# Performance work log

Measured on AMD Instinct MI355X. Metric: run time of the kernel, lower is better.

Reference implementation:

```python
import jax, jax.numpy as jnp
import numpy as np
from jax import lax

N, L, D, P, H, QK, VP = 1, 512, 256, 128, 8, 8, 8
FIN = H * P + H * VP * 7 + H * 7  # 1528: pair + value-point + beta features


def _l2g(R, t, p):
    # local_to_global: q = R @ p + t, applied over flattened point dims
    s = p.shape
    p3 = p.reshape(s[0], s[1], -1, 3)
    q = jnp.einsum('nlij,nlmj->nlmi', R, p3) + t[:, :, None, :]
    return q.reshape(s)


def _g2l(R, t, q):
    # global_to_local: p = R^T @ (q - t)
    s = q.shape
    q3 = q.reshape(s[0], s[1], -1, 3)
    p = jnp.einsum('nlji,nlmj->nlmi', R, q3 - t[:, :, None, :])
    return p.reshape(s)


def _inorm(x):  # InstanceNorm2d, affine=False, eps=1e-5, NCHW
    m = x.mean(axis=(2, 3), keepdims=True)
    v = x.var(axis=(2, 3), keepdims=True)
    return (x - m) * lax.rsqrt(v + 1e-5)


def _conv3(x, w, b):  # 3x3, stride 1, pad 1
    y = lax.conv_general_dilated(x, w, (1, 1), [(1, 1), (1, 1)],
                                 dimension_numbers=('NCHW', 'OIHW', 'NCHW'))
    return y + b[None, :, None, None]


def _ln(x, g, b):  # LayerNorm over last dim, eps=1e-5
    m = x.mean(-1, keepdims=True)
    v = x.var(-1, keepdims=True)
    return (x - m) * lax.rsqrt(v + 1e-5) * g + b


def _leaky(x):  # LeakyReLU, negative_slope=0.01
    return jnp.where(x >= 0, x, 0.01 * x)


def setup_inputs():
    key = jax.random.key(0)
    ks = jax.random.split(key, 24)
    s = 0.05
    return {
        'R': jax.random.normal(ks[0], (N, L, 3, 3), jnp.float32),
        't': jax.random.normal(ks[1], (N, L, 3), jnp.float32),
        'p_CB': jax.random.normal(ks[2], (N, L, 3), jnp.float32),
        'x': jax.random.normal(ks[3], (N, L, D), jnp.float32),
        'z': jax.random.normal(ks[4], (N, L, L, P), jnp.float32),
        'W_p2h': jax.random.normal(ks[5], (P, H), jnp.float32) * s,
        'gamma': jnp.ones((1, 1, H), jnp.float32),
        'Wq': jax.random.normal(ks[6], (D, H * QK * 3), jnp.float32) * s,
        'Wk': jax.random.normal(ks[7], (D, H * QK * 3), jnp.float32) * s,
        'Wv': jax.random.normal(ks[8], (D, H * VP * 3), jnp.float32) * s,
        'W1': jax.random.normal(ks[9], (FIN, 2 * D), jnp.float32) * s,
        'b1': jnp.zeros((2 * D,), jnp.float32),
        'ln1_g': jnp.ones((2 * D,), jnp.float32),
        'ln1_b': jnp.zeros((2 * D,), jnp.float32),
        'W2': jax.random.normal(ks[10], (2 * D, D), jnp.float32) * s,
        'b2': jnp.zeros((D,), jnp.float32),
        'ca_w': jax.random.normal(ks[11], (H, 2 * H, 3, 3), jnp.float32) * s,
        'ca_b': jnp.zeros((H,), jnp.float32),
        'ln_g': jnp.ones((D,), jnp.float32),
        'ln_b': jnp.zeros((D,), jnp.float32),
        'cp_w': jax.random.normal(ks[12], (P, H + P, 3, 3), jnp.float32) * s,
        'cp_b': jnp.zeros((P,), jnp.float32),
        'mask': jnp.ones((N, L), dtype=bool),
    }


def reference(R, t, p_CB, x, z, W_p2h, gamma, Wq, Wk, Wv, W1, b1, ln1_g, ln1_b,
              W2, b2, ca_w, ca_b, ln_g, ln_b, cp_w, cp_b, mask):
    n, l = x.shape[:2]
    # pair logits [n,l,l,H]
    logits_pair = jnp.einsum('nijp,ph->nijh', z, W_p2h)
    # spatial (point) logits: squared distances between global q/k points
    q_s = _l2g(R, t, (x @ Wq).reshape(n, l, H * QK, 3)).reshape(n, l, H, QK * 3)
    k_s = _l2g(R, t, (x @ Wk).reshape(n, l, H * QK, 3)).reshape(n, l, H, QK * 3)
    ssd = ((q_s ** 2).sum(-1)[:, :, None, :] + (k_s ** 2).sum(-1)[:, None, :, :]
           - 2.0 * jnp.einsum('nihd,njhd->nijh', q_s, k_s))
    logits_spatial = ssd * (-gamma * jnp.sqrt(2.0 / (9.0 * QK)) / 2.0)
    # conv2dalpha: InstanceNorm -> 3x3 conv -> LeakyReLU over the LxL grid
    lg = jnp.concatenate([logits_pair, logits_spatial], axis=-1).transpose(0, 3, 1, 2)
    logits_sum = _leaky(_conv3(_inorm(lg), ca_w, ca_b)).transpose(0, 2, 3, 1)
    mask_row = mask[:, :, None, None]
    mask_pair = mask_row & mask[:, None, :, None]
    logits_sum = jnp.where(mask_pair, logits_sum, logits_sum - 1e6)
    alpha = jax.nn.softmax(logits_sum, axis=2)
    alpha = jnp.where(mask_row, alpha, 0.0)
    # pair aggregation [n,l,H*P]
    feat_p2n = jnp.einsum('nijh,nijp->nihp', alpha, z).reshape(n, l, H * P)
    # spatial (value point) aggregation
    v_pts = _l2g(R, t, (x @ Wv).reshape(n, l, H, VP, 3))
    aggr = jnp.einsum('nijh,njhvc->nihvc', alpha, v_pts)
    fp = _g2l(R, t, aggr)  # [n,l,H,VP,3]
    fn = jnp.sqrt((fp ** 2).sum(-1))
    fdir = fp / (fn[..., None] + 1e-6)
    feat_spatial = jnp.concatenate(
        [fp.reshape(n, l, -1), fn.reshape(n, l, -1), fdir.reshape(n, l, -1)], -1)
    # beta (CB point) aggregation
    aggr_b = jnp.einsum('nijh,njc->nihc', alpha, p_CB)
    fpb = _g2l(R, t, aggr_b)  # [n,l,H,3]
    fnb = jnp.sqrt((fpb ** 2).sum(-1))
    fdb = fpb / (fnb[..., None] + 1e-6)
    feat_beta = jnp.concatenate([fpb.reshape(n, l, -1), fnb, fdb.reshape(n, l, -1)], -1)
    # out_transform: Linear -> LayerNorm -> LeakyReLU -> Linear
    feat_all = jnp.concatenate([feat_p2n, feat_spatial, feat_beta], -1)
    h1 = _leaky(_ln(feat_all @ W1 + b1, ln1_g, ln1_b))
    fa = h1 @ W2 + b2
    fa = jnp.where(mask[..., None], fa, 0.0)
    x_out = _ln(x + fa, ln_g, ln_b)
    # alpha2pair: InstanceNorm -> 3x3 conv -> LeakyReLU
    pz = jnp.concatenate([z, alpha], -1).transpose(0, 3, 1, 2)
    pair_out = _leaky(_conv3(_inorm(pz), cp_w, cp_b)).transpose(0, 2, 3, 1)
    return (x_out, pair_out)
```

## Files before the change

kernel.cpp:

```cpp
#include <hip/hip_runtime.h>
#include <hip/hip_bf16.h>
#include <math.h>

#define Lr 512
#define LL (512*512)
#define PZROW 73728

typedef __bf16 bf16x8 __attribute__((ext_vector_type(8)));
typedef float f32x16 __attribute__((ext_vector_type(16)));

static __device__ __forceinline__ unsigned short f2bf(float f) {
    union { float f; unsigned u; } a; a.f = f;
    unsigned r = a.u + 0x7fff + ((a.u >> 16) & 1);
    return (unsigned short)(r >> 16);
}

static __device__ __forceinline__ unsigned pack2(float lo, float hi) {
    return (unsigned)f2bf(lo) | ((unsigned)f2bf(hi) << 16);
}

__global__ __launch_bounds__(512) void zero_stats_k(float* lg_acc, float* pz_acc) {
    int t = threadIdx.x;
    if (t < 32) lg_acc[t] = 0.f;
    if (t < 272) pz_acc[t] = 0.f;
}

__global__ __launch_bounds__(256) void wb_prep_k(const float* __restrict__ cpw,
        const float* __restrict__ pzmr, unsigned short* __restrict__ wb) {
    int idx = blockIdx.x * 256 + threadIdx.x;
    if (idx >= 128 * 1296) return;
    int j = idx & 7;
    int n = (idx >> 3) & 127;
    int rest = idx >> 10;
    int lhi = rest & 1;
    int ksn = (rest >> 1) % 9;
    int tap = rest / 18;
    int c = ksn * 16 + lhi * 8 + j;
    float v = (c < 136) ? cpw[(n * 136 + c) * 9 + tap] * pzmr[c * 2 + 1] : 0.f;
    wb[idx] = f2bf(v);
}

__global__ __launch_bounds__(128) void kc_prep_k(const float* __restrict__ cpw,
        const float* __restrict__ pzmr, float* __restrict__ kc) {
    int idx = blockIdx.x * 128 + threadIdx.x;
    if (idx >= 1152) return;
    int o = idx / 9, tap = idx % 9;
    float s = 0.f;
    for (int c = 0; c < 136; c++)
        s += cpw[(o * 136 + c) * 9 + tap] * pzmr[c * 2 + 1] * pzmr[c * 2];
    kc[idx] = -s;
}

__device__ __forceinline__ const float* qkv_colptr(const float* Wq, const float* Wk, const float* Wv, int c) {
    return c < 192 ? (Wq + c) : (c < 384 ? (Wk + c - 192) : (Wv + c - 384));
}

__global__ __launch_bounds__(256) void qkv_k(const float* __restrict__ x,
        const float* __restrict__ Wq, const float* __restrict__ Wk, const float* __restrict__ Wv,
        const float* __restrict__ R, const float* __restrict__ tv,
        float* __restrict__ qs, float* __restrict__ ks, float* __restrict__ vp,
        float* __restrict__ q2, float* __restrict__ k2) {
    __shared__ float xrow[256];
    __shared__ float praw[576];
    __shared__ float tr[576];
    __shared__ float Rt[12];
    int i = blockIdx.x, t = threadIdx.x;
    xrow[t] = x[i * 256 + t];
    if (t < 12) Rt[t] = (t < 9) ? R[i * 9 + t] : tv[i * 3 + t - 9];
    __syncthreads();
    const float* p0 = qkv_colptr(Wq, Wk, Wv, t);
    const float* p1 = qkv_colptr(Wq, Wk, Wv, t + 256);
    const float* p2 = qkv_colptr(Wq, Wk, Wv, t < 64 ? t + 512 : 575);
    float a0 = 0.f, a1 = 0.f, a2 = 0.f;
    for (int f = 0; f < 256; f++) {
        float xv = xrow[f];
        a0 += xv * p0[f * 192];
        a1 += xv * p1[f * 192];
        a2 += xv * p2[f * 192];
    }
    praw[t] = a0; praw[t + 256] = a1;
    if (t < 64) praw[t + 512] = a2;
    __syncthreads();
    if (t < 192) {
        int seg = t / 64, pt = t % 64;
        float b0 = praw[seg * 192 + pt * 3], b1_ = praw[seg * 192 + pt * 3 + 1], b2_ = praw[seg * 192 + pt * 3 + 2];
        #pragma unroll
        for (int r = 0; r < 3; r++)
            tr[seg * 192 + pt * 3 + r] = Rt[r * 3] * b0 + Rt[r * 3 + 1] * b1_ + Rt[r * 3 + 2] * b2_ + Rt[9 + r];
    }
    __syncthreads();
    if (t < 8) {
        float s = 0.f;
        #pragma unroll
        for (int d = 0; d < 24; d++) { float v = tr[t * 24 + d]; s += v * v; }
        q2[i * 8 + t] = s;
    } else if (t < 16) {
        int h = t - 8; float s = 0.f;
        #pragma unroll
        for (int d = 0; d < 24; d++) { float v = tr[192 + h * 24 + d]; s += v * v; }
        k2[i * 8 + h] = s;
    }
    for (int f = t; f < 576; f += 256) {
        float v = tr[f];
        if (f < 192) qs[i * 192 + f] = v;
        else if (f < 384) ks[i * 192 + f - 192] = v;
        else vp[i * 192 + f - 384] = v;
    }
}

__global__ __launch_bounds__(256) void zstats_pzb_k(const float4* __restrict__ z4,
        float* pz_acc, unsigned short* __restrict__ pzb) {
    __shared__ float acc[256];
    int t = threadIdx.x;
    acc[t] = 0.f;
    __syncthreads();
    int chunk = t & 15, pl = t >> 4;
    int p0 = blockIdx.x * 128;
    float s[8], s2[8];
    #pragma unroll
    for (int u = 0; u < 8; u++) { s[u] = 0.f; s2[u] = 0.f; }
    #pragma unroll
    for (int k = 0; k < 8; k++) {
        int pos = p0 + k * 16 + pl;
        const float4* src = z4 + (size_t)pos * 32 + chunk * 2;
        float4 v0 = src[0], v1 = src[1];
        float vv[8] = {v0.x, v0.y, v0.z, v0.w, v1.x, v1.y, v1.z, v1.w};
        #pragma unroll
        for (int u = 0; u < 8; u++) { s[u] += vv[u]; s2[u] += vv[u] * vv[u]; }
        uint4 q;
        q.x = pack2(vv[0], vv[1]); q.y = pack2(vv[2], vv[3]);
        q.z = pack2(vv[4], vv[5]); q.w = pack2(vv[6], vv[7]);
        int row = pos >> 9, col = pos & 511;
        *(uint4*)(pzb + ((size_t)row * 18 + chunk) * 4096 + col * 8) = q;
    }
    #pragma unroll
    for (int u = 0; u < 8; u++) {
        atomicAdd(&acc[(chunk * 8 + u) * 2], s[u]);
        atomicAdd(&acc[(chunk * 8 + u) * 2 + 1], s2[u]);
    }
    __syncthreads();
    if (t < 128) {
        atomicAdd(&pz_acc[t * 2], acc[t * 2]);
        atomicAdd(&pz_acc[t * 2 + 1], acc[t * 2 + 1]);
    }
}

__global__ __launch_bounds__(256) void lg_k(const float* __restrict__ z,
        const float* __restrict__ Wp2h, const float* __restrict__ gamma,
        const float* __restrict__ qs, const float* __restrict__ ks,
        const float* __restrict__ q2, const float* __restrict__ k2,
        float* __restrict__ lg, float* lg_acc) {
    __shared__ float zl[32 * 132];
    __shared__ float wh[8 * 132];
    __shared__ float qrow[192];
    __shared__ float q2row[8];
    __shared__ float sacc[32];
    int i = blockIdx.x, t = threadIdx.x;
    for (int f = t; f < 1024; f += 256) { int h = f >> 7, p = f & 127; wh[h * 132 + p] = Wp2h[p * 8 + h]; }
    if (t < 192) qrow[t] = qs[i * 192 + t];
    if (t < 8) q2row[t] = q2[i * 8 + t];
    if (t < 32) sacc[t] = 0.f;
    int jl = t >> 3, h = t & 7;
    float gsc = -gamma[h] * 0.08333333333333333f;
    float sp = 0.f, sp2 = 0.f, ss = 0.f, ss2 = 0.f;
    __syncthreads();
    for (int jt = 0; jt < 16; jt++) {
        int j0 = jt * 32;
        const float4* zsrc = (const float4*)(z + (size_t)(i * 512 + j0) * 128);
        #pragma unroll
        for (int r = 0; r < 4; r++) {
            int idx4 = r * 256 + t;
            int zjl = idx4 >> 5, p4 = idx4 & 31;
            *(float4*)&zl[zjl * 132 + p4 * 4] = zsrc[idx4];
        }
        __syncthreads();
        int j = j0 + jl;
        float accp = 0.f;
        const float4* za = (const float4*)&zl[jl * 132];
        const float4* wa = (const float4*)&wh[h * 132];
        #pragma unroll
        for (int p4 = 0; p4 < 32; p4++) {
            float4 a = za[p4], b = wa[p4];
            accp += a.x * b.x + a.y * b.y + a.z * b.z + a.w * b.w;
        }
        const float4* kp = (const float4*)(ks + (size_t)j * 192 + h * 24);
        const float4* qp = (const float4*)&qrow[h * 24];
        float dqk = 0.f;
        #pragma unroll
        for (int d4 = 0; d4 < 6; d4++) {
            float4 a = qp[d4], b = kp[d4];
            dqk += a.x * b.x + a.y * b.y + a.z * b.z + a.w * b.w;
        }
        float ssd = q2row[h] + k2[j * 8 + h] - 2.f * dqk;
        float lgs = ssd * gsc;
        lg[(size_t)h * LL + i * 512 + j] = accp;
        lg[(size_t)(8 + h) * LL + i * 512 + j] = lgs;
        sp += accp; sp2 += accp * accp; ss += lgs; ss2 += lgs * lgs;
        __syncthreads();
    }
    atomicAdd(&sacc[h * 2], sp);        atomicAdd(&sacc[h * 2 + 1], sp2);
    atomicAdd(&sacc[16 + h * 2], ss);   atomicAdd(&sacc[16 + h * 2 + 1], ss2);
    __syncthreads();
    if (t < 16) {
        atomicAdd(&lg_acc[t * 2], sacc[t * 2]);
        atomicAdd(&lg_acc[t * 2 + 1], sacc[t * 2 + 1]);
    }
}

__global__ void finalize_k(const float* __restrict__ acc, float* __restrict__ mr, int nch, float npix) {
    int t = threadIdx.x;
    if (t < nch) {
        float m = acc[t * 2] / npix;
        float v = acc[t * 2 + 1] / npix - m * m;
        mr[t * 2] = m;
        mr[t * 2 + 1] = rsqrtf(fmaxf(v, 0.f) + 1e-5f);
    }
}

__global__ __launch_bounds__(256) void ca_softmax_k(const float* __restrict__ lg,
        const float* __restrict__ lgmr, const float* __restrict__ caw, const float* __restrict__ cab,
        float* __restrict__ alpha, float* pz_acc, unsigned short* __restrict__ pzb) {
    __shared__ float wl[1152];
    __shared__ float mr[32];
    __shared__ float cb[8];
    __shared__ float red[64];
    int i = blockIdx.x, t = threadIdx.x;
    for (int f = t; f < 1152; f += 256) {
        int o = f & 7, k = f >> 3; int c = k / 9, r = k % 9;
        wl[f] = caw[(o * 16 + c) * 9 + r];
    }
    if (t < 32) mr[t] = lgmr[t];
    if (t < 8) cb[t] = cab[t];
    __syncthreads();
    float acc0[8], acc1[8];
    #pragma unroll
    for (int o = 0; o < 8; o++) { acc0[o] = 0.f; acc1[o] = 0.f; }
    int j0 = t, j1 = t + 256;
    const float4* w4 = (const float4*)wl;
    for (int c = 0; c < 16; c++) {
        float m = mr[c * 2], rs = mr[c * 2 + 1];
        const float* lgc = lg + (size_t)c * LL;
        #pragma unroll
        for (int di = 0; di < 3; di++) {
            int row = i - 1 + di;
            if (row < 0 || row >= 512) continue;
            const float* lr = lgc + (size_t)row * 512;
            float v0[3], v1[3];
            v0[0] = (j0 > 0) ? (lr[j0 - 1] - m) * rs : 0.f;
            v0[1] = (lr[j0] - m) * rs;
            v0[2] = (lr[j0 + 1] - m) * rs;
            v1[0] = (lr[j1 - 1] - m) * rs;
            v1[1] = (lr[j1] - m) * rs;
            v1[2] = (j1 < 511) ? (lr[j1 + 1] - m) * rs : 0.f;
            int wb = (c * 9 + di * 3) * 2;
            #pragma unroll
            for (int dj = 0; dj < 3; dj++) {
                float4 wa = w4[wb + dj * 2], wbv = w4[wb + dj * 2 + 1];
                acc0[0] += wa.x * v0[dj]; acc0[1] += wa.y * v0[dj]; acc0[2] += wa.z * v0[dj]; acc0[3] += wa.w * v0[dj];
                acc0[4] += wbv.x * v0[dj]; acc0[5] += wbv.y * v0[dj]; acc0[6] += wbv.z * v0[dj]; acc0[7] += wbv.w * v0[dj];
                acc1[0] += wa.x * v1[dj]; acc1[1] += wa.y * v1[dj]; acc1[2] += wa.z * v1[dj]; acc1[3] += wa.w * v1[dj];
                acc1[4] += wbv.x * v1[dj]; acc1[5] += wbv.y * v1[dj]; acc1[6] += wbv.z * v1[dj]; acc1[7] += wbv.w * v1[dj];
            }
        }
    }
    float s0[8], s1[8];
    #pragma unroll
    for (int o = 0; o < 8; o++) {
        float v = acc0[o] + cb[o]; s0[o] = v >= 0.f ? v : 0.01f * v;
        float w = acc1[o] + cb[o]; s1[o] = w >= 0.f ? w : 0.01f * w;
    }
    int lane = t & 63, wid = t >> 6;
    float mx[8];
    #pragma unroll
    for (int o = 0; o < 8; o++) mx[o] = fmaxf(s0[o], s1[o]);
    for (int off = 1; off < 64; off <<= 1) {
        #pragma unroll
        for (int o = 0; o < 8; o++) mx[o] = fmaxf(mx[o], __shfl_xor(mx[o], off));
    }
    if (lane == 0) {
        #pragma unroll
        for (int o = 0; o < 8; o++) red[wid * 8 + o] = mx[o];
    }
    __syncthreads();
    float M[8];
    #pragma unroll
    for (int o = 0; o < 8; o++) M[o] = fmaxf(fmaxf(red[o], red[8 + o]), fmaxf(red[16 + o], red[24 + o]));
    float e0[8], e1[8], sm[8];
    #pragma unroll
    for (int o = 0; o < 8; o++) { e0[o] = expf(s0[o] - M[o]); e1[o] = expf(s1[o] - M[o]); sm[o] = e0[o] + e1[o]; }
    __syncthreads();
    for (int off = 1; off < 64; off <<= 1) {
        #pragma unroll
        for (int o = 0; o < 8; o++) sm[o] += __shfl_xor(sm[o], off);
    }
    if (lane == 0) {
        #pragma unroll
        for (int o = 0; o < 8; o++) red[wid * 8 + o] = sm[o];
    }
    __syncthreads();
    float a0[8], a1[8], st_s[8], st_q[8];
    #pragma unroll
    for (int o = 0; o < 8; o++) {
        float rden = 1.f / (red[o] + red[8 + o] + red[16 + o] + red[24 + o]);
        a0[o] = e0[o] * rden; a1[o] = e1[o] * rden;
        st_s[o] = a0[o] + a1[o];
        st_q[o] = a0[o] * a0[o] + a1[o] * a1[o];
    }
    size_t base = (size_t)i * 512;
    #pragma unroll
    for (int o = 0; o < 8; o++) {
        alpha[(size_t)o * LL + base + t] = a0[o];
        alpha[(size_t)o * LL + base + t + 256] = a1[o];
    }
    {
        uint4 p0, p1;
        p0.x = pack2(a0[0], a0[1]); p0.y = pack2(a0[2], a0[3]);
        p0.z = pack2(a0[4], a0[5]); p0.w = pack2(a0[6], a0[7]);
        p1.x = pack2(a1[0], a1[1]); p1.y = pack2(a1[2], a1[3]);
        p1.z = pack2(a1[4], a1[5]); p1.w = pack2(a1[6], a1[7]);
        unsigned short* pb = pzb + (size_t)i * PZROW + 16 * 4096;
        *(uint4*)(pb + (size_t)t * 8) = p0;
        *(uint4*)(pb + (size_t)(t + 256) * 8) = p1;
        uint4 zz = {0u, 0u, 0u, 0u};
        *(uint4*)(pb + 4096 + (size_t)t * 8) = zz;
        *(uint4*)(pb + 4096 + (size_t)(t + 256) * 8) = zz;
    }
    __syncthreads();
    for (int off = 1; off < 64; off <<= 1) {
        #pragma unroll
        for (int o = 0; o < 8; o++) { st_s[o] += __shfl_xor(st_s[o], off); st_q[o] += __shfl_xor(st_q[o], off); }
    }
    if (lane == 0) {
        #pragma unroll
        for (int o = 0; o < 8; o++) { red[wid * 8 + o] = st_s[o]; red[32 + wid * 8 + o] = st_q[o]; }
    }
    __syncthreads();
    if (t < 8) {
        float ts = red[t] + red[8 + t] + red[16 + t] + red[24 + t];
        float tq = red[32 + t] + red[40 + t] + red[48 + t] + red[56 + t];
        atomicAdd(&pz_acc[(128 + t) * 2], ts);
        atomicAdd(&pz_acc[(128 + t) * 2 + 1], tq);
    }
}

__global__ __launch_bounds__(256) void feat_mlp_k(
        const float* __restrict__ alpha, const float* __restrict__ z,
        const float* __restrict__ vp, const float* __restrict__ pcb,
        const float* __restrict__ R, const float* __restrict__ tv,
        const float* __restrict__ W1, const float* __restrict__ b1,
        const float* __restrict__ ln1g, const float* __restrict__ ln1b,
        const float* __restrict__ W2, const float* __restrict__ b2,
        const float* __restrict__ lng, const float* __restrict__ lnb,
        const float* __restrict__ x, float* __restrict__ xout) {
    __shared__ float al[8 * 512];
    __shared__ float zl[64 * 128];
    __shared__ float feat[1536];
    __shared__ float h1[512];
    __shared__ float agg[216];
    __shared__ float Rt[12];
    __shared__ float redl[8];
    int i = blockIdx.x, t = threadIdx.x;
    for (int f = t; f < 4096; f += 256) al[f] = alpha[(size_t)(f >> 9) * LL + i * 512 + (f & 511)];
    if (t < 12) Rt[t] = (t < 9) ? R[i * 9 + t] : tv[i * 3 + t - 9];
    __syncthreads();
    if (t < 216) {
        float a = 0.f;
        if (t < 192) {
            int h = t / 24;
            const float* vptr = vp + t;
            const float* ar = al + h * 512;
            for (int j = 0; j < 512; j++) a += ar[j] * vptr[(size_t)j * 192];
        } else {
            int u = t - 192; int h = u / 3, cc = u % 3;
            const float* ar = al + h * 512;
            for (int j = 0; j < 512; j++) a += ar[j] * pcb[j * 3 + cc];
        }
        agg[t] = a;
    }
    float4 accp = {0.f, 0.f, 0.f, 0.f};
    int hh = t >> 5, p4 = t & 31;
    for (int jc = 0; jc < 8; jc++) {
        const float4* zsrc = (const float4*)(z + (size_t)(i * 512 + jc * 64) * 128);
        #pragma unroll
        for (int r = 0; r < 8; r++) ((float4*)zl)[r * 256 + t] = zsrc[r * 256 + t];
        __syncthreads();
        const float* ar = al + hh * 512 + jc * 64;
        const float4* zv = (const float4*)zl + p4;
        #pragma unroll 4
        for (int jl = 0; jl < 64; jl++) {
            float a = ar[jl];
            float4 v = zv[jl * 32];
            accp.x += a * v.x; accp.y += a * v.y; accp.z += a * v.z; accp.w += a * v.w;
        }
        __syncthreads();
    }
    *(float4*)&feat[hh * 128 + p4 * 4] = accp;
    __syncthreads();
    if (t < 64) {
        int h = t >> 3, v = t & 7;
        float d0 = agg[h * 24 + v * 3] - Rt[9];
        float d1 = agg[h * 24 + v * 3 + 1] - Rt[10];
        float d2 = agg[h * 24 + v * 3 + 2] - Rt[11];
        float f0 = Rt[0] * d0 + Rt[3] * d1 + Rt[6] * d2;
        float f1 = Rt[1] * d0 + Rt[4] * d1 + Rt[7] * d2;
        float f2 = Rt[2] * d0 + Rt[5] * d1 + Rt[8] * d2;
        float n = sqrtf(f0 * f0 + f1 * f1 + f2 * f2);
        float rn = 1.f / (n + 1e-6f);
        feat[1024 + h * 24 + v * 3] = f0;
        feat[1024 + h * 24 + v * 3 + 1] = f1;
        feat[1024 + h * 24 + v * 3 + 2] = f2;
        feat[1216 + h * 8 + v] = n;
        feat[1280 + h * 24 + v * 3] = f0 * rn;
        feat[1280 + h * 24 + v * 3 + 1] = f1 * rn;
        feat[1280 + h * 24 + v * 3 + 2] = f2 * rn;
    } else if (t < 72) {
        int h = t - 64;
        float d0 = agg[192 + h * 3] - Rt[9];
        float d1 = agg[192 + h * 3 + 1] - Rt[10];
        float d2 = agg[192 + h * 3 + 2] - Rt[11];
        float f0 = Rt[0] * d0 + Rt[3] * d1 + Rt[6] * d2;
        float f1 = Rt[1] * d0 + Rt[4] * d1 + Rt[7] * d2;
        float f2 = Rt[2] * d0 + Rt[5] * d1 + Rt[8] * d2;
        float n = sqrtf(f0 * f0 + f1 * f1 + f2 * f2);
        float rn = 1.f / (n + 1e-6f);
        feat[1472 + h * 3] = f0; feat[1472 + h * 3 + 1] = f1; feat[1472 + h * 3 + 2] = f2;
        feat[1496 + h] = n;
        feat[1504 + h * 3] = f0 * rn; feat[1504 + h * 3 + 1] = f1 * rn; feat[1504 + h * 3 + 2] = f2 * rn;
    }
    __syncthreads();
    float acc0 = b1[t], acc1 = b1[t + 256];
    const float4* f4 = (const float4*)feat;
    for (int f = 0; f < 1528; f += 4) {
        float4 fv = f4[f >> 2];
        const float* w = W1 + (size_t)f * 512 + t;
        acc0 += fv.x * w[0] + fv.y * w[512] + fv.z * w[1024] + fv.w * w[1536];
        const float* w2p = w + 256;
        acc1 += fv.x * w2p[0] + fv.y * w2p[512] + fv.z * w2p[1024] + fv.w * w2p[1536];
    }
    int lane = t & 63, wid = t >> 6;
    float s = acc0 + acc1, s2 = acc0 * acc0 + acc1 * acc1;
    for (int off = 1; off < 64; off <<= 1) { s += __shfl_xor(s, off); s2 += __shfl_xor(s2, off); }
    if (lane == 0) { redl[wid * 2] = s; redl[wid * 2 + 1] = s2; }
    __syncthreads();
    float S = redl[0] + redl[2] + redl[4] + redl[6];
    float S2 = redl[1] + redl[3] + redl[5] + redl[7];
    float mean = S / 512.f;
    float rstd = rsqrtf(fmaxf(S2 / 512.f - mean * mean, 0.f) + 1e-5f);
    float hv0 = (acc0 - mean) * rstd * ln1g[t] + ln1b[t];
    float hv1 = (acc1 - mean) * rstd * ln1g[t + 256] + ln1b[t + 256];
    hv0 = hv0 >= 0.f ? hv0 : 0.01f * hv0;
    hv1 = hv1 >= 0.f ? hv1 : 0.01f * hv1;
    h1[t] = hv0; h1[t + 256] = hv1;
    __syncthreads();
    float a2 = b2[t];
    const float4* h14 = (const float4*)h1;
    for (int k = 0; k < 512; k += 4) {
        float4 hv = h14[k >> 2];
        const float* w = W2 + (size_t)k * 256 + t;
        a2 += hv.x * w[0] + hv.y * w[256] + hv.z * w[512] + hv.w * w[768];
    }
    float xv = x[i * 256 + t] + a2;
    float ss_ = xv, sq_ = xv * xv;
    for (int off = 1; off < 64; off <<= 1) { ss_ += __shfl_xor(ss_, off); sq_ += __shfl_xor(sq_, off); }
    __syncthreads();
    if (lane == 0) { redl[wid * 2] = ss_; redl[wid * 2 + 1] = sq_; }
    __syncthreads();
    float Sx = redl[0] + redl[2] + redl[4] + redl[6];
    float Sx2 = redl[1] + redl[3] + redl[5] + redl[7];
    float mx = Sx / 256.f;
    float rsx = rsqrtf(fmaxf(Sx2 / 256.f - mx * mx, 0.f) + 1e-5f);
    xout[i * 256 + t] = (xv - mx) * rsx * lng[t] + lnb[t];
}

__global__ __launch_bounds__(256) void conv_mfma_k(
        const unsigned short* __restrict__ pzb, const unsigned short* __restrict__ wb,
        const float* __restrict__ kc, const float* __restrict__ cpb,
        float* __restrict__ pout) {
    __shared__ unsigned short abuf[2368 * 8];
    __shared__ float csA[128];
    __shared__ float cs0[128];
    __shared__ float cs2[128];
    int t = threadIdx.x;
    int bid = blockIdx.x;
    int swz = (bid & 7) * 256 + (bid >> 3);
    int i = swz >> 2;
    int j0 = (swz & 3) * 128;
    if (t < 128) {
        int o = t;
        float a0 = 0.f, a1 = 0.f, a2 = 0.f;
        #pragma unroll
        for (int di = 0; di < 3; di++) {
            int grow = i - 1 + di;
            if (grow < 0 || grow > 511) continue;
            a0 += kc[o * 9 + di * 3];
            a1 += kc[o * 9 + di * 3 + 1];
            a2 += kc[o * 9 + di * 3 + 2];
        }
        cs0[o] = a0; cs2[o] = a2; csA[o] = cpb[o] + a0 + a1 + a2;
    }
    int w = t >> 6, lane = t & 63;
    int l31 = lane & 31, lhi = lane >> 5;
    int mt0 = (w & 1) * 64;
    int nt0 = (w >> 1) * 64;

    uint4 rg[10];
    #define STAGE_LOAD(DI) do {                                                \
        int grow_ = i - 1 + (DI);                                              \
        bool rowok_ = (grow_ >= 0 && grow_ < 512);                             \
        const unsigned short* rowp_ = pzb + (size_t)grow_ * PZROW;             \
        _Pragma("unroll")                                                      \
        for (int k = 0; k < 10; k++) {                                         \
            int f_ = t + k * 256;                                              \
            uint4 v_ = {0u, 0u, 0u, 0u};                                       \
            if (f_ < 2340) {                                                   \
                int c_ = f_ / 130, col_ = f_ - c_ * 130;                       \
                int gcol_ = j0 - 1 + col_;                                     \
                if (rowok_ && (unsigned)gcol_ < 512u)                          \
                    v_ = *(const uint4*)(rowp_ + c_ * 4096 + gcol_ * 8);       \
            }                                                                  \
            rg[k] = v_;                                                        \
        }                                                                      \
    } while (0)

    #define STAGE_WRITE() do {                                                 \
        _Pragma("unroll")                                                      \
        for (int k = 0; k < 10; k++) {                                         \
            int f_ = t + k * 256;                                              \
            if (f_ < 2340) *(uint4*)(abuf + f_ * 8) = rg[k];                   \
        }                                                                      \
    } while (0)

    f32x16 acc00 = {}, acc01 = {}, acc10 = {}, acc11 = {};

    STAGE_LOAD(0);
    STAGE_WRITE();
    __syncthreads();

    #pragma unroll
    for (int di = 0; di < 3; di++) {
        if (di < 2) STAGE_LOAD(di + 1);
        #pragma unroll
        for (int dj = 0; dj < 3; dj++) {
            int tap = di * 3 + dj;
            const unsigned short* wt = wb + (size_t)(tap * 18 + lhi) * 1024 + (nt0 + l31) * 8;
            const unsigned short* ap0 = abuf + lhi * 1040 + (mt0 + l31 + dj) * 8;
            const unsigned short* ap1 = ap0 + 256;
            #pragma unroll
            for (int ksn = 0; ksn < 9; ksn++) {
                bf16x8 a0 = *(const bf16x8*)(ap0 + ksn * 2080);
                bf16x8 a1 = *(const bf16x8*)(ap1 + ksn * 2080);
                bf16x8 b0 = *(const bf16x8*)(wt + ksn * 2048);
                bf16x8 b1 = *(const bf16x8*)(wt + ksn * 2048 + 256);
                acc00 = __builtin_amdgcn_mfma_f32_32x32x16_bf16(a0, b0, acc00, 0, 0, 0);
                acc01 = __builtin_amdgcn_mfma_f32_32x32x16_bf16(a0, b1, acc01, 0, 0, 0);
                acc10 = __builtin_amdgcn_mfma_f32_32x32x16_bf16(a1, b0, acc10, 0, 0, 0);
                acc11 = __builtin_amdgcn_mfma_f32_32x32x16_bf16(a1, b1, acc11, 0, 0, 0);
            }
        }
        __syncthreads();
        if (di < 2) {
            STAGE_WRITE();
            __syncthreads();
        }
    }
    #undef STAGE_LOAD
    #undef STAGE_WRITE

    float* fb = (float*)abuf;
    #pragma unroll
    for (int mh = 0; mh < 2; mh++) {
        if ((w & 1) == mh) {
            #pragma unroll
            for (int mi = 0; mi < 2; mi++) {
                #pragma unroll
                for (int ni = 0; ni < 2; ni++) {
                    const f32x16* a = (mi == 0) ? (ni == 0 ? &acc00 : &acc01) : (ni == 0 ? &acc10 : &acc11);
                    int nb = nt0 + ni * 32 + l31;
                    float bA = csA[nb], b0_ = cs0[nb], b2_ = cs2[nb];
                    #pragma unroll
                    for (int r = 0; r < 16; r++) {
                        int ml = mi * 32 + 4 * lhi + (r & 3) + 8 * (r >> 2);
                        int j = j0 + mh * 64 + ml;
                        float bias = bA - (j == 0 ? b0_ : 0.f) - (j == 511 ? b2_ : 0.f);
                        float v = (*a)[r] + bias;
                        v = v >= 0.f ? v : 0.01f * v;
                        fb[ml * 128 + nb] = v;
                    }
                }
            }
        }
        __syncthreads();
        const float4* fb4 = (const float4*)fb;
        float4* gdst = (float4*)(pout + ((size_t)(i * 512 + j0 + mh * 64)) * 128);
        #pragma unroll
        for (int k = 0; k < 8; k++) {
            int f4i = k * 256 + t;
            gdst[f4i] = fb4[f4i];
        }
        __syncthreads();
    }
}

extern "C" void kernel_launch(void* const* d_in, const int* in_sizes, int n_in,
                              void* d_out, int out_size, void* d_ws, size_t ws_size,
                              hipStream_t stream) {
    (void)in_sizes; (void)n_in; (void)out_size; (void)ws_size;
    const float* R    = (const float*)d_in[0];
    const float* tv   = (const float*)d_in[1];
    const float* pcb  = (const float*)d_in[2];
    const float* x    = (const float*)d_in[3];
    const float* z    = (const float*)d_in[4];
    const float* wp2h = (const float*)d_in[5];
    const float* gamma= (const float*)d_in[6];
    const float* Wq   = (const float*)d_in[7];
    const float* Wk   = (const float*)d_in[8];
    const float* Wv   = (const float*)d_in[9];
    const float* W1   = (const float*)d_in[10];
    const float* b1   = (const float*)d_in[11];
    const float* ln1g = (const float*)d_in[12];
    const float* ln1b = (const float*)d_in[13];
    const float* W2   = (const float*)d_in[14];
    const float* b2   = (const float*)d_in[15];
    const float* caw  = (const float*)d_in[16];
    const float* cab  = (const float*)d_in[17];
    const float* lng  = (const float*)d_in[18];
    const float* lnb  = (const float*)d_in[19];
    const float* cpw  = (const float*)d_in[20];
    const float* cpb  = (const float*)d_in[21];

    float* ws = (float*)d_ws;
    float* qs     = ws;
    float* ksv    = qs + 98304;
    float* vp     = ksv + 98304;
    float* q2     = vp + 98304;
    float* k2     = q2 + 4096;
    float* lg_acc = k2 + 4096;
    float* lg_mr  = lg_acc + 32;
    float* pz_acc = lg_mr + 32;
    float* pz_mr  = pz_acc + 272;
    float* kc     = pz_mr + 272;
    unsigned short* wbq = (unsigned short*)(kc + 1152);
    float* lg     = kc + 1152 + 82944;
    float* alpha  = lg + 16 * LL;
    unsigned short* pzb = (unsigned short*)(alpha + 8 * LL);

    float* xout = (float*)d_out;
    float* pout = xout + 131072;

    hipLaunchKernelGGL(zero_stats_k, dim3(1), dim3(512), 0, stream, lg_acc, pz_acc);
    hipLaunchKernelGGL(qkv_k, dim3(512), dim3(256), 0, stream, x, Wq, Wk, Wv, R, tv, qs, ksv, vp, q2, k2);
    hipLaunchKernelGGL(zstats_pzb_k, dim3(2048), dim3(256), 0, stream, (const float4*)z, pz_acc, pzb);
    hipLaunchKernelGGL(lg_k, dim3(512), dim3(256), 0, stream, z, wp2h, gamma, qs, ksv, q2, k2, lg, lg_acc);
    hipLaunchKernelGGL(finalize_k, dim3(1), dim3(64), 0, stream, lg_acc, lg_mr, 16, 262144.f);
    hipLaunchKernelGGL(ca_softmax_k, dim3(512), dim3(256), 0, stream, lg, lg_mr, caw, cab, alpha, pz_acc, pzb);
    hipLaunchKernelGGL(finalize_k, dim3(1), dim3(192), 0, stream, pz_acc, pz_mr, 136, 262144.f);
    hipLaunchKernelGGL(wb_prep_k, dim3(648), dim3(256), 0, stream, cpw, pz_mr, wbq);
    hipLaunchKernelGGL(kc_prep_k, dim3(9), dim3(128), 0, stream, cpw, pz_mr, kc);
    hipLaunchKernelGGL(feat_mlp_k, dim3(512), dim3(256), 0, stream,
                       alpha, z, vp, pcb, R, tv, W1, b1, ln1g, ln1b, W2, b2, lng, lnb, x, xout);
    hipLaunchKernelGGL(conv_mfma_k, dim3(2048), dim3(256), 0, stream, pzb, wbq, kc, cpb, pout);
}
```

Before: 773.7 us.

## Process two rows per block in feat MLP with bf16 transposed W1

The feature+MLP kernel now handles two query rows per 512-thread block, so each W1 weight load serves both rows. W1 is pre-converted each call into a bf16, k-interleaved layout, which halves weight traffic and allows 16-byte vector loads. The z aggregation now reads global memory directly instead of staging through shared memory. The costs are bf16 rounding of W1 (a precision risk), an extra prep kernel and workspace, and half as many blocks.

```diff
diff --git a/kernel.cpp b/kernel.cpp
--- a/kernel.cpp
+++ b/kernel.cpp
@@ -17,6 +17,13 @@
 
 static __device__ __forceinline__ unsigned pack2(float lo, float hi) {
     return (unsigned)f2bf(lo) | ((unsigned)f2bf(hi) << 16);
+}
+
+static __device__ __forceinline__ float bflo(unsigned u) {
+    union { unsigned u; float f; } c; c.u = u << 16; return c.f;
+}
+static __device__ __forceinline__ float bfhi(unsigned u) {
+    union { unsigned u; float f; } c; c.u = u & 0xffff0000u; return c.f;
 }
 
 __global__ __launch_bounds__(512) void zero_stats_k(float* lg_acc, float* pz_acc) {
@@ -38,6 +45,16 @@
     int c = ksn * 16 + lhi * 8 + j;
     float v = (c < 136) ? cpw[(n * 136 + c) * 9 + tap] * pzmr[c * 2 + 1] : 0.f;
     wb[idx] = f2bf(v);
+}
+
+__global__ __launch_bounds__(256) void w1t_prep_k(const float* __restrict__ W1,
+        unsigned short* __restrict__ w1t) {
+    int idx = blockIdx.x * 256 + threadIdx.x;
+    if (idx >= 782336) return;
+    int s = idx & 7;
+    int t = (idx >> 3) & 511;
+    int k8 = idx >> 12;
+    w1t[idx] = f2bf(W1[(size_t)(k8 * 8 + s) * 512 + t]);
 }
 
 __global__ __launch_bounds__(128) void kc_prep_k(const float* __restrict__ cpw,
@@ -343,78 +360,87 @@
     }
 }
 
-__global__ __launch_bounds__(256) void feat_mlp_k(
+__global__ __launch_bounds__(512) void feat_mlp2_k(
         const float* __restrict__ alpha, const float* __restrict__ z,
         const float* __restrict__ vp, const float* __restrict__ pcb,
         const float* __restrict__ R, const float* __restrict__ tv,
-        const float* __restrict__ W1, const float* __restrict__ b1,
+        const unsigned short* __restrict__ w1t, const float* __restrict__ b1,
         const float* __restrict__ ln1g, const float* __restrict__ ln1b,
         const float* __restrict__ W2, const float* __restrict__ b2,
         const float* __restrict__ lng, const float* __restrict__ lnb,
         const float* __restrict__ x, float* __restrict__ xout) {
-    __shared__ float al[8 * 512];
-    __shared__ float zl[64 * 128];
-    __shared__ float feat[1536];
-    __shared__ float h1[512];
-    __shared__ float agg[216];
-    __shared__ float Rt[12];
-    __shared__ float redl[8];
-    int i = blockIdx.x, t = threadIdx.x;
-    for (int f = t; f < 4096; f += 256) al[f] = alpha[(size_t)(f >> 9) * LL + i * 512 + (f & 511)];
-    if (t < 12) Rt[t] = (t < 9) ? R[i * 9 + t] : tv[i * 3 + t - 9];
-    __syncthreads();
-    if (t < 216) {
-        float a = 0.f;
-        if (t < 192) {
-            int h = t / 24;
-            const float* vptr = vp + t;
-            const float* ar = al + h * 512;
-            for (int j = 0; j < 512; j++) a += ar[j] * vptr[(size_t)j * 192];
+    __shared__ float al2[2][4096];
+    __shared__ float feat2[2][1536];
+    __shared__ float h1l[2][512];
+    __shared__ float agg2[2][216];
+    __shared__ float Rt2[2][12];
+    __shared__ float redl[32];
+    int t = threadIdx.x;
+    int i0 = blockIdx.x * 2;
+    for (int f = t; f < 2048; f += 512) {
+        int r = f >> 10, q = f & 1023;
+        ((float4*)al2[r])[q] =
+            ((const float4*)(alpha + (size_t)(q >> 7) * LL + (size_t)(i0 + r) * 512))[q & 127];
+    }
+    if (t < 24) { int r = t / 12, u = t % 12; Rt2[r][u] = (u < 9) ? R[(i0 + r) * 9 + u] : tv[(i0 + r) * 3 + u - 9]; }
+    __syncthreads();
+    {
+        int r = t >> 8, hh = (t >> 5) & 7, p4 = t & 31;
+        const float4* zr4 = (const float4*)z + (size_t)(i0 + r) * 512 * 32 + p4;
+        const float* ar = al2[r] + hh * 512;
+        float4 accp = {0.f, 0.f, 0.f, 0.f};
+        #pragma unroll 8
+        for (int j = 0; j < 512; j++) {
+            float a = ar[j];
+            float4 v = zr4[(size_t)j * 32];
+            accp.x += a * v.x; accp.y += a * v.y; accp.z += a * v.z; accp.w += a * v.w;
+        }
+        *(float4*)&feat2[r][hh * 128 + p4 * 4] = accp;
+    }
+    if (t < 432) {
+        int rr = t / 216, u = t - (t / 216) * 216;
+        const float* ar;
+        float acc = 0.f;
+        if (u < 192) {
+            int h = u / 24;
+            ar = al2[rr] + h * 512;
+            #pragma unroll 4
+            for (int j = 0; j < 512; j++) acc += ar[j] * vp[(size_t)j * 192 + u];
         } else {
-            int u = t - 192; int h = u / 3, cc = u % 3;
-            const float* ar = al + h * 512;
-            for (int j = 0; j < 512; j++) a += ar[j] * pcb[j * 3 + cc];
-        }
-        agg[t] = a;
-    }
-    float4 accp = {0.f, 0.f, 0.f, 0.f};
-    int hh = t >> 5, p4 = t & 31;
-    for (int jc = 0; jc < 8; jc++) {
-        const float4* zsrc = (const float4*)(z + (size_t)(i * 512 + jc * 64) * 128);
-        #pragma unroll
-        for (int r = 0; r < 8; r++) ((float4*)zl)[r * 256 + t] = zsrc[r * 256 + t];
-        __syncthreads();
-        const float* ar = al + hh * 512 + jc * 64;
-        const float4* zv = (const float4*)zl + p4;
-        #pragma unroll 4
-        for (int jl = 0; jl < 64; jl++) {
-            float a = ar[jl];
-            float4 v = zv[jl * 32];
-            accp.x += a * v.x; accp.y += a * v.y; accp.z += a * v.z; accp.w += a * v.w;
-        }
-        __syncthreads();
-    }
-    *(float4*)&feat[hh * 128 + p4 * 4] = accp;
-    __syncthreads();
-    if (t < 64) {
-        int h = t >> 3, v = t & 7;
-        float d0 = agg[h * 24 + v * 3] - Rt[9];
-        float d1 = agg[h * 24 + v * 3 + 1] - Rt[10];
-        float d2 = agg[h * 24 + v * 3 + 2] - Rt[11];
+            int v_ = u - 192; int h = v_ / 3, cc = v_ % 3;
+            ar = al2[rr] + h * 512;
+            #pragma unroll 4
+            for (int j = 0; j < 512; j++) acc += ar[j] * pcb[j * 3 + cc];
+        }
+        agg2[rr][u] = acc;
+    }
+    __syncthreads();
+    if (t < 128) {
+        int rr = t >> 6, idx = t & 63;
+        int h = idx >> 3, vv = idx & 7;
+        const float* Rt = Rt2[rr];
+        float* feat = feat2[rr];
+        const float* agg = agg2[rr];
+        float d0 = agg[h * 24 + vv * 3] - Rt[9];
+        float d1 = agg[h * 24 + vv * 3 + 1] - Rt[10];
+        float d2 = agg[h * 24 + vv * 3 + 2] - Rt[11];
         float f0 = Rt[0] * d0 + Rt[3] * d1 + Rt[6] * d2;
         float f1 = Rt[1] * d0 + Rt[4] * d1 + Rt[7] * d2;
         float f2 = Rt[2] * d0 + Rt[5] * d1 + Rt[8] * d2;
         float n = sqrtf(f0 * f0 + f1 * f1 + f2 * f2);
         float rn = 1.f / (n + 1e-6f);
-        feat[1024 + h * 24 + v * 3] = f0;
-        feat[1024 + h * 24 + v * 3 + 1] = f1;
-        feat[1024 + h * 24 + v * 3 + 2] = f2;
-        feat[1216 + h * 8 + v] = n;
-        feat[1280 + h * 24 + v * 3] = f0 * rn;
-        feat[1280 + h * 24 + v * 3 + 1] = f1 * rn;
-        feat[1280 + h * 24 + v * 3 + 2] = f2 * rn;
-    } else if (t < 72) {
-        int h = t - 64;
+        feat[1024 + h * 24 + vv * 3] = f0;
+        feat[1024 + h * 24 + vv * 3 + 1] = f1;
+        feat[1024 + h * 24 + vv * 3 + 2] = f2;
+        feat[1216 + h * 8 + vv] = n;
+        feat[1280 + h * 24 + vv * 3] = f0 * rn;
+        feat[1280 + h * 24 + vv * 3 + 1] = f1 * rn;
+        feat[1280 + h * 24 + vv * 3 + 2] = f2 * rn;
+    } else if (t < 144) {
+        int u = t - 128; int rr = u >> 3, h = u & 7;
+        const float* Rt = Rt2[rr];
+        float* feat = feat2[rr];
+        const float* agg = agg2[rr];
         float d0 = agg[192 + h * 3] - Rt[9];
         float d1 = agg[192 + h * 3 + 1] - Rt[10];
         float d2 = agg[192 + h * 3 + 2] - Rt[11];
@@ -428,48 +454,69 @@
         feat[1504 + h * 3] = f0 * rn; feat[1504 + h * 3 + 1] = f1 * rn; feat[1504 + h * 3 + 2] = f2 * rn;
     }
     __syncthreads();
-    float acc0 = b1[t], acc1 = b1[t + 256];
-    const float4* f4 = (const float4*)feat;
-    for (int f = 0; f < 1528; f += 4) {
-        float4 fv = f4[f >> 2];
-        const float* w = W1 + (size_t)f * 512 + t;
-        acc0 += fv.x * w[0] + fv.y * w[512] + fv.z * w[1024] + fv.w * w[1536];
-        const float* w2p = w + 256;
-        acc1 += fv.x * w2p[0] + fv.y * w2p[512] + fv.z * w2p[1024] + fv.w * w2p[1536];
+    float acc0 = b1[t], acc1 = acc0;
+    {
+        const float4* f40 = (const float4*)feat2[0];
+        const float4* f41 = (const float4*)feat2[1];
+        const uint4* wp = (const uint4*)(w1t + (size_t)t * 8);
+        #pragma unroll 4
+        for (int k8 = 0; k8 < 191; k8++) {
+            uint4 wv = wp[(size_t)k8 * 512];
+            float w0 = bflo(wv.x), w1 = bfhi(wv.x);
+            float w2 = bflo(wv.y), w3 = bfhi(wv.y);
+            float w4 = bflo(wv.z), w5 = bfhi(wv.z);
+            float w6 = bflo(wv.w), w7 = bfhi(wv.w);
+            float4 fa0 = f40[k8 * 2], fb0 = f40[k8 * 2 + 1];
+            float4 fa1 = f41[k8 * 2], fb1 = f41[k8 * 2 + 1];
+            acc0 += fa0.x * w0 + fa0.y * w1 + fa0.z * w2 + fa0.w * w3
+                  + fb0.x * w4 + fb0.y * w5 + fb0.z * w6 + fb0.w * w7;
+            acc1 += fa1.x * w0 + fa1.y * w1 + fa1.z * w2 + fa1.w * w3
+                  + fb1.x * w4 + fb1.y * w5 + fb1.z * w6 + fb1.w * w7;
+        }
     }
     int lane = t & 63, wid = t >> 6;
-    float s = acc0 + acc1, s2 = acc0 * acc0 + acc1 * acc1;
-    for (int off = 1; off < 64; off <<= 1) { s += __shfl_xor(s, off); s2 += __shfl_xor(s2, off); }
-    if (lane == 0) { redl[wid * 2] = s; redl[wid * 2 + 1] = s2; }
-    __syncthreads();
-    float S = redl[0] + redl[2] + redl[4] + redl[6];
-    float S2 = redl[1] + redl[3] + redl[5] + redl[7];
-    float mean = S / 512.f;
-    float rstd = rsqrtf(fmaxf(S2 / 512.f - mean * mean, 0.f) + 1e-5f);
-    float hv0 = (acc0 - mean) * rstd * ln1g[t] + ln1b[t];
-    float hv1 = (acc1 - mean) * rstd * ln1g[t + 256] + ln1b[t + 256];
-    hv0 = hv0 >= 0.f ? hv0 : 0.01f * hv0;
-    hv1 = hv1 >= 0.f ? hv1 : 0.01f * hv1;
-    h1[t] = hv0; h1[t + 256] = hv1;
-    __syncthreads();
-    float a2 = b2[t];
-    const float4* h14 = (const float4*)h1;
-    for (int k = 0; k < 512; k += 4) {
-        float4 hv = h14[k >> 2];
-        const float* w = W2 + (size_t)k * 256 + t;
-        a2 += hv.x * w[0] + hv.y * w[256] + hv.z * w[512] + hv.w * w[768];
-    }
-    float xv = x[i * 256 + t] + a2;
-    float ss_ = xv, sq_ = xv * xv;
-    for (int off = 1; off < 64; off <<= 1) { ss_ += __shfl_xor(ss_, off); sq_ += __shfl_xor(sq_, off); }
-    __syncthreads();
-    if (lane == 0) { redl[wid * 2] = ss_; redl[wid * 2 + 1] = sq_; }
-    __syncthreads();
-    float Sx = redl[0] + redl[2] + redl[4] + redl[6];
-    float Sx2 = redl[1] + redl[3] + redl[5] + redl[7];
-    float mx = Sx / 256.f;
-    float rsx = rsqrtf(fmaxf(Sx2 / 256.f - mx * mx, 0.f) + 1e-5f);
-    xout[i * 256 + t] = (xv - mx) * rsx * lng[t] + lnb[t];
+    {
+        float s0 = acc0, q0 = acc0 * acc0, s1 = acc1, q1 = acc1 * acc1;
+        for (int off = 1; off < 64; off <<= 1) {
+            s0 += __shfl_xor(s0, off); q0 += __shfl_xor(q0, off);
+            s1 += __shfl_xor(s1, off); q1 += __shfl_xor(q1, off);
+        }
+        if (lane == 0) { redl[wid * 4] = s0; redl[wid * 4 + 1] = q0; redl[wid * 4 + 2] = s1; redl[wid * 4 + 3] = q1; }
+        __syncthreads();
+        float S0 = 0.f, Q0 = 0.f, S1 = 0.f, Q1 = 0.f;
+        #pragma unroll
+        for (int w_ = 0; w_ < 8; w_++) { S0 += redl[w_ * 4]; Q0 += redl[w_ * 4 + 1]; S1 += redl[w_ * 4 + 2]; Q1 += redl[w_ * 4 + 3]; }
+        float m0 = S0 / 512.f, r0 = rsqrtf(fmaxf(Q0 / 512.f - m0 * m0, 0.f) + 1e-5f);
+        float m1 = S1 / 512.f, r1 = rsqrtf(fmaxf(Q1 / 512.f - m1 * m1, 0.f) + 1e-5f);
+        float g = ln1g[t], bb = ln1b[t];
+        float h0 = (acc0 - m0) * r0 * g + bb; h0 = h0 >= 0.f ? h0 : 0.01f * h0;
+        float h1_ = (acc1 - m1) * r1 * g + bb; h1_ = h1_ >= 0.f ? h1_ : 0.01f * h1_;
+        h1l[0][t] = h0; h1l[1][t] = h1_;
+    }
+    __syncthreads();
+    int r2 = t >> 8, c = t & 255;
+    float a2 = b2[c];
+    {
+        const float4* h4 = (const float4*)h1l[r2];
+        #pragma unroll 4
+        for (int k = 0; k < 512; k += 4) {
+            float4 hv = h4[k >> 2];
+            const float* w = W2 + (size_t)k * 256 + c;
+            a2 += hv.x * w[0] + hv.y * w[256] + hv.z * w[512] + hv.w * w[768];
+        }
+    }
+    float xv = x[(size_t)(i0 + r2) * 256 + c] + a2;
+    {
+        float ss = xv, qq = xv * xv;
+        for (int off = 1; off < 64; off <<= 1) { ss += __shfl_xor(ss, off); qq += __shfl_xor(qq, off); }
+        __syncthreads();
+        if (lane == 0) { redl[wid * 2] = ss; redl[wid * 2 + 1] = qq; }
+        __syncthreads();
+        float Sx = redl[r2 * 8] + redl[r2 * 8 + 2] + redl[r2 * 8 + 4] + redl[r2 * 8 + 6];
+        float Qx = redl[r2 * 8 + 1] + redl[r2 * 8 + 3] + redl[r2 * 8 + 5] + redl[r2 * 8 + 7];
+        float mx = Sx / 256.f, rsx = rsqrtf(fmaxf(Qx / 256.f - mx * mx, 0.f) + 1e-5f);
+        xout[(size_t)(i0 + r2) * 256 + c] = (xv - mx) * rsx * lng[c] + lnb[c];
+    }
 }
 
 __global__ __launch_bounds__(256) void conv_mfma_k(
@@ -640,7 +687,8 @@
     float* pz_mr  = pz_acc + 272;
     float* kc     = pz_mr + 272;
     unsigned short* wbq = (unsigned short*)(kc + 1152);
-    float* lg     = kc + 1152 + 82944;
+    unsigned short* w1t = wbq + 165888;
+    float* lg     = kc + 1152 + 82944 + 391168;
     float* alpha  = lg + 16 * LL;
     unsigned short* pzb = (unsigned short*)(alpha + 8 * LL);
 
@@ -648,6 +696,7 @@
     float* pout = xout + 131072;
 
     hipLaunchKernelGGL(zero_stats_k, dim3(1), dim3(512), 0, stream, lg_acc, pz_acc);
+    hipLaunchKernelGGL(w1t_prep_k, dim3(3056), dim3(256), 0, stream, W1, w1t);
     hipLaunchKernelGGL(qkv_k, dim3(512), dim3(256), 0, stream, x, Wq, Wk, Wv, R, tv, qs, ksv, vp, q2, k2);
     hipLaunchKernelGGL(zstats_pzb_k, dim3(2048), dim3(256), 0, stream, (const float4*)z, pz_acc, pzb);
     hipLaunchKernelGGL(lg_k, dim3(512), dim3(256), 0, stream, z, wp2h, gamma, qs, ksv, q2, k2, lg, lg_acc);
@@ -656,7 +705,7 @@
     hipLaunchKernelGGL(finalize_k, dim3(1), dim3(192), 0, stream, pz_acc, pz_mr, 136, 262144.f);
     hipLaunchKernelGGL(wb_prep_k, dim3(648), dim3(256), 0, stream, cpw, pz_mr, wbq);
     hipLaunchKernelGGL(kc_prep_k, dim3(9), dim3(128), 0, stream, cpw, pz_mr, kc);
-    hipLaunchKernelGGL(feat_mlp_k, dim3(512), dim3(256), 0, stream,
-                       alpha, z, vp, pcb, R, tv, W1, b1, ln1g, ln1b, W2, b2, lng, lnb, x, xout);
+    hipLaunchKernelGGL(feat_mlp2_k, dim3(256), dim3(512), 0, stream,
+                       alpha, z, vp, pcb, R, tv, w1t, b1, ln1g, ln1b, W2, b2, lng, lnb, x, xout);
     hipLaunchKernelGGL(conv_mfma_k, dim3(2048), dim3(256), 0, stream, pzb, wbq, kc, cpb, pout);
 }
```

Result: faster. 753.2 us (-2.6%).
